# Kernel tuning notes

Measured on AMD Instinct MI355X. Metric: run time of the kernel, lower is better.

Reference implementation:

```python
import jax, jax.numpy as jnp
import numpy as np

H, W = 1080, 1920
MAX_POINTS = 2048
MIN_DEPTH, MAX_DEPTH = 0.1, 2.0
# module sets intrinsics to None (bug); use realistic 1080p pinhole intrinsics
FX = 1050.0
FY = 1050.0
CX = W / 2.0
CY = H / 2.0


def setup_inputs() -> dict:
    key = jax.random.key(0)
    k1, k2 = jax.random.split(key)
    # depth in [0.2, 1.8] m so every pixel passes the validity filter
    depth_image = 0.2 + 1.6 * jax.random.uniform(k1, (H, W), dtype=jnp.float32)
    rgb_image = 255.0 * jax.random.uniform(k2, (H, W, 3), dtype=jnp.float32)
    return {"depth_image": depth_image, "rgb_image": rgb_image}


def _fps_indices(xyz, m):
    """Iterative furthest point sampling. xyz: [N,3] -> [m] int32 indices."""
    N = xyz.shape[0]
    first = jnp.array(0, dtype=jnp.int32)
    init_dists = jnp.full((N,), jnp.inf, dtype=jnp.float32)

    def body(carry, _):
        dists, last = carry
        p = xyz[last]                                 # [3]
        d = jnp.sum((xyz - p) ** 2, axis=1)           # [N]
        dists = jnp.minimum(dists, d)
        nxt = jnp.argmax(dists).astype(jnp.int32)
        return (dists, nxt), nxt

    _, rest = jax.lax.scan(body, (init_dists, first), None, length=m - 1)
    return jnp.concatenate([first[None], rest])


def reference(depth_image, rgb_image):
    # depth -> xyz  [H*W, 3]
    u, v = jnp.meshgrid(jnp.arange(W), jnp.arange(H), indexing='xy')
    u = u.reshape(-1).astype(jnp.float32)
    v = v.reshape(-1).astype(jnp.float32)
    depth = depth_image.reshape(-1)
    xyz = jnp.stack([(u - CX) * depth / FX,
                     (v - CY) * depth / FY,
                     depth], axis=1)                  # [N, 3]
    rgb = rgb_image.reshape(-1, 3) / 255.0            # [N, 3]

    # validity filter (invalid -> inf xyz, 0 rgb), as in the source
    valid = ((depth > MIN_DEPTH) & (depth < MAX_DEPTH)
             & (depth > 0) & jnp.isfinite(depth))
    vm = valid[:, None]
    valid_xyz = jnp.where(vm, xyz, jnp.inf)
    valid_rgb = jnp.where(vm, rgb, 0.0)

    # FPS sampling (N >= max_points branch)
    idx = _fps_indices(valid_xyz.astype(jnp.float32), MAX_POINTS)  # [M]
    sampled_xyz = valid_xyz[idx]                      # [M, 3]
    sampled_rgb = valid_rgb[idx]                      # [M, 3]

    # coordinate normalization to [0,1]
    xyz_min = jnp.min(sampled_xyz, axis=0, keepdims=True)
    centered = sampled_xyz - xyz_min
    xyz_max = jnp.max(centered, axis=0, keepdims=True)
    xyz_max = jnp.where(xyz_max < 1e-8, 1.0, xyz_max)
    XYZ = centered / xyz_max

    return jnp.concatenate([sampled_xyz, sampled_rgb, XYZ], axis=1)  # [M, 9]
```

## Files before the change

kernel.cpp:

```cpp
#include <hip/hip_runtime.h>
#include <math.h>

#define HH   1080
#define WW   1920
#define NPIX (HH*WW)
#define MAXP 2048
#define NTHR 512
#define NWAVE (NTHR/64)
#define PPB  8192
#define KPT  16
#define NBLK 254

#define CXF 960.0f
#define CYF 540.0f
#define FXF 1050.0f
#define FYF 1050.0f

__device__ unsigned long long g_packed[2 * NBLK];
__device__ unsigned long long g_win[2];

__device__ __forceinline__ float proj_x(float u, float d) {
    return __fdiv_rn(__fmul_rn(__fsub_rn(u, CXF), d), FXF);
}
__device__ __forceinline__ float proj_y(float v, float d) {
    return __fdiv_rn(__fmul_rn(__fsub_rn(v, CYF), d), FYF);
}
__device__ __forceinline__ unsigned long long umax64(unsigned long long a, unsigned long long b) {
    return a > b ? a : b;
}

__global__ void zero_ws_kernel() {
    unsigned i = threadIdx.x;
    if (i < 2u * NBLK) g_packed[i] = 0ull;
    if (i < 2u)        g_win[i]    = 0ull;
}

#define FOR16(M)  M(0) M(1) M(2) M(3) M(4) M(5) M(6) M(7) M(8) M(9) M(10) M(11) M(12) M(13) M(14) M(15)
#define FOR16D(M) M(15) M(14) M(13) M(12) M(11) M(10) M(9) M(8) M(7) M(6) M(5) M(4) M(3) M(2) M(1) M(0)
#define DECLD(j) float D##j;

#define UPDJ(j) { \
    unsigned o = tid + j##u * (unsigned)NTHR; \
    float4 P = sP[o]; \
    float dx = __fsub_rn(P.x, px); \
    float dy = __fsub_rn(P.y, py); \
    float dz = __fsub_rn(P.z, pz); \
    float s  = __fadd_rn(__fadd_rn(__fmul_rn(dx, dx), __fmul_rn(dy, dy)), __fmul_rn(dz, dz)); \
    float nd = fminf(D##j, s); \
    D##j = nd; \
    if (nd >= bestd) { bestd = nd; besti = base + o; } }

__global__ __attribute__((amdgpu_flat_work_group_size(NTHR, NTHR)))
void fps_kernel(const float* __restrict__ depth, const float* __restrict__ rgb,
                float* __restrict__ out)
{
    const unsigned tid  = threadIdx.x;
    const unsigned lane = threadIdx.x & 63u;
    const unsigned wid  = threadIdx.x >> 6;
    const unsigned blk  = blockIdx.x;
    const float FINF = __int_as_float(0x7f800000);

    __shared__ float4 sP[PPB];
    __shared__ unsigned long long s_pp[NWAVE];
    __shared__ unsigned long long s_win;
    __shared__ unsigned           s_widx[MAXP];

    if (blk == (unsigned)NBLK) {
        if (wid == 0) {
            if (lane == 0) s_widx[0] = 0u;
            const bool has3 = (lane + 192u) < (unsigned)NBLK;
            for (int it = 1; it < MAXP; ++it) {
                const unsigned long long tag = (unsigned long long)it;
                const unsigned long long* row = &g_packed[(size_t)(it & 1) * NBLK];
                unsigned long long v0, v1, v2, v3 = 0ull;
                for (;;) {
                    v0 = __hip_atomic_load(row + lane,        __ATOMIC_RELAXED, __HIP_MEMORY_SCOPE_AGENT);
                    v1 = __hip_atomic_load(row + lane + 64u,  __ATOMIC_RELAXED, __HIP_MEMORY_SCOPE_AGENT);
                    v2 = __hip_atomic_load(row + lane + 128u, __ATOMIC_RELAXED, __HIP_MEMORY_SCOPE_AGENT);
                    if (has3)
                        v3 = __hip_atomic_load(row + lane + 192u, __ATOMIC_RELAXED, __HIP_MEMORY_SCOPE_AGENT);
                    if ((v0 >> 53) == tag && (v1 >> 53) == tag && (v2 >> 53) == tag &&
                        (!has3 || (v3 >> 53) == tag)) break;
                    __builtin_amdgcn_s_sleep(1);
                }
                unsigned long long w = umax64(umax64(v0, v1), umax64(v2, v3));
                #pragma unroll
                for (int off = 32; off; off >>= 1) w = umax64(w, __shfl_xor(w, off));
                unsigned widx = 0x1FFFFFu - (unsigned)(w & 0x1FFFFFull);
                if (lane == 0) {
                    float wd = depth[widx];
                    s_widx[it] = widx;
                    __hip_atomic_store(&g_win[it & 1],
                        (tag << 53) |
                        ((unsigned long long)__float_as_uint(wd) << 21) |
                        (unsigned long long)(0x1FFFFFu - widx),
                        __ATOMIC_RELAXED, __HIP_MEMORY_SCOPE_AGENT);
                }
            }
        }
        __syncthreads();

        float ex[4], ey[4], ez[4], er[4], eg[4], eb[4];
        #pragma unroll
        for (int q = 0; q < 4; ++q) {
            int i = (int)tid + q * NTHR;
            unsigned sidx = s_widx[i];
            float d = depth[sidx];
            float u = (float)(sidx % WW);
            float v = (float)(sidx / WW);
            bool val = (d > 0.1f) && (d < 2.0f) && __builtin_isfinite(d);
            ex[q] = val ? proj_x(u, d) : FINF;
            ey[q] = val ? proj_y(v, d) : FINF;
            ez[q] = val ? d : FINF;
            er[q] = val ? __fdiv_rn(rgb[3u * sidx + 0u], 255.0f) : 0.0f;
            eg[q] = val ? __fdiv_rn(rgb[3u * sidx + 1u], 255.0f) : 0.0f;
            eb[q] = val ? __fdiv_rn(rgb[3u * sidx + 2u], 255.0f) : 0.0f;
        }
        float mn[3], mx[3];
        mn[0] = fminf(fminf(ex[0], ex[1]), fminf(ex[2], ex[3]));
        mx[0] = fmaxf(fmaxf(ex[0], ex[1]), fmaxf(ex[2], ex[3]));
        mn[1] = fminf(fminf(ey[0], ey[1]), fminf(ey[2], ey[3]));
        mx[1] = fmaxf(fmaxf(ey[0], ey[1]), fmaxf(ey[2], ey[3]));
        mn[2] = fminf(fminf(ez[0], ez[1]), fminf(ez[2], ez[3]));
        mx[2] = fmaxf(fmaxf(ez[0], ez[1]), fmaxf(ez[2], ez[3]));
        #pragma unroll
        for (int c = 0; c < 3; ++c) {
            for (int off = 32; off > 0; off >>= 1) {
                mn[c] = fminf(mn[c], __shfl_xor(mn[c], off));
                mx[c] = fmaxf(mx[c], __shfl_xor(mx[c], off));
            }
        }
        __shared__ float s_mn[NWAVE][3], s_mx[NWAVE][3];
        __shared__ float f_mn[3], f_sc[3];
        if (lane == 0) {
            for (int c = 0; c < 3; ++c) { s_mn[wid][c] = mn[c]; s_mx[wid][c] = mx[c]; }
        }
        __syncthreads();
        if (wid == 0) {
            float a[3], b[3];
            for (int c = 0; c < 3; ++c) {
                a[c] = (lane < NWAVE) ? s_mn[lane][c] : FINF;
                b[c] = (lane < NWAVE) ? s_mx[lane][c] : -FINF;
            }
            for (int off = NWAVE / 2; off > 0; off >>= 1) {
                for (int c = 0; c < 3; ++c) {
                    a[c] = fminf(a[c], __shfl_xor(a[c], off));
                    b[c] = fmaxf(b[c], __shfl_xor(b[c], off));
                }
            }
            if (lane == 0) {
                for (int c = 0; c < 3; ++c) {
                    f_mn[c] = a[c];
                    float m = __fsub_rn(b[c], a[c]);
                    f_sc[c] = (m < 1e-8f) ? 1.0f : m;
                }
            }
        }
        __syncthreads();
        float MN0 = f_mn[0], MN1 = f_mn[1], MN2 = f_mn[2];
        float SC0 = f_sc[0], SC1 = f_sc[1], SC2 = f_sc[2];
        #pragma unroll
        for (int q = 0; q < 4; ++q) {
            int i = (int)tid + q * NTHR;
            out[9 * i + 0] = ex[q];
            out[9 * i + 1] = ey[q];
            out[9 * i + 2] = ez[q];
            out[9 * i + 3] = er[q];
            out[9 * i + 4] = eg[q];
            out[9 * i + 5] = eb[q];
            out[9 * i + 6] = __fdiv_rn(__fsub_rn(ex[q], MN0), SC0);
            out[9 * i + 7] = __fdiv_rn(__fsub_rn(ey[q], MN1), SC1);
            out[9 * i + 8] = __fdiv_rn(__fsub_rn(ez[q], MN2), SC2);
        }
        return;
    }

    const unsigned base = blk << 13;

    FOR16(DECLD)

    #define INITJ(j) { \
        unsigned o   = tid + j##u * (unsigned)NTHR; \
        unsigned idx = base + o; \
        float x, y, z; \
        if (idx < NPIX) { \
            float d = depth[idx]; \
            float u = (float)(idx % WW); \
            float v = (float)(idx / WW); \
            bool val = (d > 0.1f) && (d < 2.0f) && __builtin_isfinite(d); \
            x = val ? proj_x(u, d) : FINF; \
            y = val ? proj_y(v, d) : FINF; \
            z = val ? d : FINF; \
            D##j = FINF; \
        } else { x = 0.f; y = 0.f; z = 0.f; D##j = -1.0f; } \
        sP[o] = make_float4(x, y, z, 0.0f); }
    FOR16(INITJ)
    if (tid == 0) s_win = 0ull;
    __syncthreads();

    float px, py, pz;
    {
        float d = depth[0];
        bool val = (d > 0.1f) && (d < 2.0f) && __builtin_isfinite(d);
        px = val ? proj_x(0.0f, d) : FINF;
        py = val ? proj_y(0.0f, d) : FINF;
        pz = val ? d : FINF;
    }

    for (int it = 1; it < MAXP; ++it) {
        const unsigned long long tag = (unsigned long long)it;

        float bestd = -2.0f;
        unsigned besti = 0u;
        FOR16D(UPDJ)

        unsigned long long pk =
            (tag << 53) |
            ((unsigned long long)__float_as_uint(bestd) << 21) |
            (unsigned long long)(0x1FFFFFu - besti);

        #pragma unroll
        for (int off = 32; off; off >>= 1) pk = umax64(pk, __shfl_xor(pk, off));
        if (lane == 0) s_pp[wid] = pk;
        __syncthreads();

        if (wid == 0 && lane == 0) {
            unsigned long long p2 = s_pp[0];
            #pragma unroll
            for (int k = 1; k < NWAVE; ++k) p2 = umax64(p2, s_pp[k]);
            __hip_atomic_store(&g_packed[(size_t)(it & 1) * NBLK + blk], p2,
                               __ATOMIC_RELAXED, __HIP_MEMORY_SCOPE_AGENT);
        }

        if (it == MAXP - 1) break;

        if (wid == 0 && lane == 0) {
            unsigned long long gv;
            for (;;) {
                gv = __hip_atomic_load(&g_win[it & 1], __ATOMIC_RELAXED, __HIP_MEMORY_SCOPE_AGENT);
                if ((gv >> 53) == tag) break;
            }
            __hip_atomic_store(&s_win, gv, __ATOMIC_RELAXED, __HIP_MEMORY_SCOPE_WORKGROUP);
        }
        unsigned long long gv;
        for (;;) {
            gv = __hip_atomic_load(&s_win, __ATOMIC_RELAXED, __HIP_MEMORY_SCOPE_WORKGROUP);
            if ((gv >> 53) == tag) break;
        }

        unsigned widx = 0x1FFFFFu - (unsigned)(gv & 0x1FFFFFull);
        float    wd   = __uint_as_float((unsigned)((gv >> 21) & 0xFFFFFFFFull));

        float uu = (float)(widx % WW);
        float vv = (float)(widx / WW);
        bool val = (wd > 0.1f) && (wd < 2.0f) && __builtin_isfinite(wd);
        px = val ? proj_x(uu, wd) : FINF;
        py = val ? proj_y(vv, wd) : FINF;
        pz = val ? wd : FINF;
    }
}

extern "C" void kernel_launch(void* const* d_in, const int* in_sizes, int n_in,
                              void* d_out, int out_size, void* d_ws, size_t ws_size,
                              hipStream_t stream) {
    const float* depth = (const float*)d_in[0];
    const float* rgb   = (const float*)d_in[1];
    float* out = (float*)d_out;

    zero_ws_kernel<<<dim3(1), dim3(512), 0, stream>>>();

    void* args[] = { (void*)&depth, (void*)&rgb, (void*)&out };
    hipLaunchCooperativeKernel((const void*)fps_kernel, dim3(NBLK + 1), dim3(NTHR),
                               args, 0, stream);
}
```

Measured before the change: 6.493 ms.

## Remove coordinator block; each block reduces global argmax redundantly

Drops the dedicated reducer block and the global winner broadcast. Instead, wave 0 of every block polls all per-block partial maxima, reduces them itself, and publishes the winner through shared memory. Block 0 also records the sampled indices and writes the output at the end. This removes one global round-trip per iteration (partials to coordinator, then winner back to all blocks), at the cost of every block reading all partials each iteration, which adds L2 polling traffic.

```diff
diff --git a/kernel.cpp b/kernel.cpp
--- a/kernel.cpp
+++ b/kernel.cpp
@@ -17,7 +17,6 @@
 #define FYF 1050.0f
 
 __device__ unsigned long long g_packed[2 * NBLK];
-__device__ unsigned long long g_win[2];
 
 __device__ __forceinline__ float proj_x(float u, float d) {
     return __fdiv_rn(__fmul_rn(__fsub_rn(u, CXF), d), FXF);
@@ -32,7 +31,6 @@
 __global__ void zero_ws_kernel() {
     unsigned i = threadIdx.x;
     if (i < 2u * NBLK) g_packed[i] = 0ull;
-    if (i < 2u)        g_win[i]    = 0ull;
 }
 
 #define FOR16(M)  M(0) M(1) M(2) M(3) M(4) M(5) M(6) M(7) M(8) M(9) M(10) M(11) M(12) M(13) M(14) M(15)
@@ -58,124 +56,13 @@
     const unsigned lane = threadIdx.x & 63u;
     const unsigned wid  = threadIdx.x >> 6;
     const unsigned blk  = blockIdx.x;
+    const unsigned base = blk << 13;
     const float FINF = __int_as_float(0x7f800000);
 
     __shared__ float4 sP[PPB];
     __shared__ unsigned long long s_pp[NWAVE];
     __shared__ unsigned long long s_win;
     __shared__ unsigned           s_widx[MAXP];
-
-    if (blk == (unsigned)NBLK) {
-        if (wid == 0) {
-            if (lane == 0) s_widx[0] = 0u;
-            const bool has3 = (lane + 192u) < (unsigned)NBLK;
-            for (int it = 1; it < MAXP; ++it) {
-                const unsigned long long tag = (unsigned long long)it;
-                const unsigned long long* row = &g_packed[(size_t)(it & 1) * NBLK];
-                unsigned long long v0, v1, v2, v3 = 0ull;
-                for (;;) {
-                    v0 = __hip_atomic_load(row + lane,        __ATOMIC_RELAXED, __HIP_MEMORY_SCOPE_AGENT);
-                    v1 = __hip_atomic_load(row + lane + 64u,  __ATOMIC_RELAXED, __HIP_MEMORY_SCOPE_AGENT);
-                    v2 = __hip_atomic_load(row + lane + 128u, __ATOMIC_RELAXED, __HIP_MEMORY_SCOPE_AGENT);
-                    if (has3)
-                        v3 = __hip_atomic_load(row + lane + 192u, __ATOMIC_RELAXED, __HIP_MEMORY_SCOPE_AGENT);
-                    if ((v0 >> 53) == tag && (v1 >> 53) == tag && (v2 >> 53) == tag &&
-                        (!has3 || (v3 >> 53) == tag)) break;
-                    __builtin_amdgcn_s_sleep(1);
-                }
-                unsigned long long w = umax64(umax64(v0, v1), umax64(v2, v3));
-                #pragma unroll
-                for (int off = 32; off; off >>= 1) w = umax64(w, __shfl_xor(w, off));
-                unsigned widx = 0x1FFFFFu - (unsigned)(w & 0x1FFFFFull);
-                if (lane == 0) {
-                    float wd = depth[widx];
-                    s_widx[it] = widx;
-                    __hip_atomic_store(&g_win[it & 1],
-                        (tag << 53) |
-                        ((unsigned long long)__float_as_uint(wd) << 21) |
-                        (unsigned long long)(0x1FFFFFu - widx),
-                        __ATOMIC_RELAXED, __HIP_MEMORY_SCOPE_AGENT);
-                }
-            }
-        }
-        __syncthreads();
-
-        float ex[4], ey[4], ez[4], er[4], eg[4], eb[4];
-        #pragma unroll
-        for (int q = 0; q < 4; ++q) {
-            int i = (int)tid + q * NTHR;
-            unsigned sidx = s_widx[i];
-            float d = depth[sidx];
-            float u = (float)(sidx % WW);
-            float v = (float)(sidx / WW);
-            bool val = (d > 0.1f) && (d < 2.0f) && __builtin_isfinite(d);
-            ex[q] = val ? proj_x(u, d) : FINF;
-            ey[q] = val ? proj_y(v, d) : FINF;
-            ez[q] = val ? d : FINF;
-            er[q] = val ? __fdiv_rn(rgb[3u * sidx + 0u], 255.0f) : 0.0f;
-            eg[q] = val ? __fdiv_rn(rgb[3u * sidx + 1u], 255.0f) : 0.0f;
-            eb[q] = val ? __fdiv_rn(rgb[3u * sidx + 2u], 255.0f) : 0.0f;
-        }
-        float mn[3], mx[3];
-        mn[0] = fminf(fminf(ex[0], ex[1]), fminf(ex[2], ex[3]));
-        mx[0] = fmaxf(fmaxf(ex[0], ex[1]), fmaxf(ex[2], ex[3]));
-        mn[1] = fminf(fminf(ey[0], ey[1]), fminf(ey[2], ey[3]));
-        mx[1] = fmaxf(fmaxf(ey[0], ey[1]), fmaxf(ey[2], ey[3]));
-        mn[2] = fminf(fminf(ez[0], ez[1]), fminf(ez[2], ez[3]));
-        mx[2] = fmaxf(fmaxf(ez[0], ez[1]), fmaxf(ez[2], ez[3]));
-        #pragma unroll
-        for (int c = 0; c < 3; ++c) {
-            for (int off = 32; off > 0; off >>= 1) {
-                mn[c] = fminf(mn[c], __shfl_xor(mn[c], off));
-                mx[c] = fmaxf(mx[c], __shfl_xor(mx[c], off));
-            }
-        }
-        __shared__ float s_mn[NWAVE][3], s_mx[NWAVE][3];
-        __shared__ float f_mn[3], f_sc[3];
-        if (lane == 0) {
-            for (int c = 0; c < 3; ++c) { s_mn[wid][c] = mn[c]; s_mx[wid][c] = mx[c]; }
-        }
-        __syncthreads();
-        if (wid == 0) {
-            float a[3], b[3];
-            for (int c = 0; c < 3; ++c) {
-                a[c] = (lane < NWAVE) ? s_mn[lane][c] : FINF;
-                b[c] = (lane < NWAVE) ? s_mx[lane][c] : -FINF;
-            }
-            for (int off = NWAVE / 2; off > 0; off >>= 1) {
-                for (int c = 0; c < 3; ++c) {
-                    a[c] = fminf(a[c], __shfl_xor(a[c], off));
-                    b[c] = fmaxf(b[c], __shfl_xor(b[c], off));
-                }
-            }
-            if (lane == 0) {
-                for (int c = 0; c < 3; ++c) {
-                    f_mn[c] = a[c];
-                    float m = __fsub_rn(b[c], a[c]);
-                    f_sc[c] = (m < 1e-8f) ? 1.0f : m;
-                }
-            }
-        }
-        __syncthreads();
-        float MN0 = f_mn[0], MN1 = f_mn[1], MN2 = f_mn[2];
-        float SC0 = f_sc[0], SC1 = f_sc[1], SC2 = f_sc[2];
-        #pragma unroll
-        for (int q = 0; q < 4; ++q) {
-            int i = (int)tid + q * NTHR;
-            out[9 * i + 0] = ex[q];
-            out[9 * i + 1] = ey[q];
-            out[9 * i + 2] = ez[q];
-            out[9 * i + 3] = er[q];
-            out[9 * i + 4] = eg[q];
-            out[9 * i + 5] = eb[q];
-            out[9 * i + 6] = __fdiv_rn(__fsub_rn(ex[q], MN0), SC0);
-            out[9 * i + 7] = __fdiv_rn(__fsub_rn(ey[q], MN1), SC1);
-            out[9 * i + 8] = __fdiv_rn(__fsub_rn(ez[q], MN2), SC2);
-        }
-        return;
-    }
-
-    const unsigned base = blk << 13;
 
     FOR16(DECLD)
 
@@ -195,7 +82,7 @@
         } else { x = 0.f; y = 0.f; z = 0.f; D##j = -1.0f; } \
         sP[o] = make_float4(x, y, z, 0.0f); }
     FOR16(INITJ)
-    if (tid == 0) s_win = 0ull;
+    if (tid == 0) { s_win = 0ull; s_widx[0] = 0u; }
     __syncthreads();
 
     float px, py, pz;
@@ -207,6 +94,8 @@
         pz = val ? d : FINF;
     }
 
+    const bool has3 = (lane + 192u) < (unsigned)NBLK;
+
     for (int it = 1; it < MAXP; ++it) {
         const unsigned long long tag = (unsigned long long)it;
 
@@ -232,24 +121,65 @@
                                __ATOMIC_RELAXED, __HIP_MEMORY_SCOPE_AGENT);
         }
 
-        if (it == MAXP - 1) break;
-
-        if (wid == 0 && lane == 0) {
+        if (it == MAXP - 1) {
+            if (blk == 0 && wid == 0) {
+                const unsigned long long* row = &g_packed[(size_t)(it & 1) * NBLK];
+                unsigned long long v0, v1, v2, v3 = 0ull;
+                for (;;) {
+                    v0 = __hip_atomic_load(row + lane,        __ATOMIC_RELAXED, __HIP_MEMORY_SCOPE_AGENT);
+                    v1 = __hip_atomic_load(row + lane + 64u,  __ATOMIC_RELAXED, __HIP_MEMORY_SCOPE_AGENT);
+                    v2 = __hip_atomic_load(row + lane + 128u, __ATOMIC_RELAXED, __HIP_MEMORY_SCOPE_AGENT);
+                    if (has3)
+                        v3 = __hip_atomic_load(row + lane + 192u, __ATOMIC_RELAXED, __HIP_MEMORY_SCOPE_AGENT);
+                    if ((v0 >> 53) == tag && (v1 >> 53) == tag && (v2 >> 53) == tag &&
+                        (!has3 || (v3 >> 53) == tag)) break;
+                    __builtin_amdgcn_s_sleep(1);
+                }
+                unsigned long long w = umax64(umax64(v0, v1), umax64(v2, v3));
+                #pragma unroll
+                for (int off = 32; off; off >>= 1) w = umax64(w, __shfl_xor(w, off));
+                if (lane == 0) s_widx[it] = 0x1FFFFFu - (unsigned)(w & 0x1FFFFFull);
+            }
+            break;
+        }
+
+        unsigned widx; float wd;
+        if (wid == 0) {
+            const unsigned long long* row = &g_packed[(size_t)(it & 1) * NBLK];
+            unsigned long long v0, v1, v2, v3 = 0ull;
+            for (;;) {
+                v0 = __hip_atomic_load(row + lane,        __ATOMIC_RELAXED, __HIP_MEMORY_SCOPE_AGENT);
+                v1 = __hip_atomic_load(row + lane + 64u,  __ATOMIC_RELAXED, __HIP_MEMORY_SCOPE_AGENT);
+                v2 = __hip_atomic_load(row + lane + 128u, __ATOMIC_RELAXED, __HIP_MEMORY_SCOPE_AGENT);
+                if (has3)
+                    v3 = __hip_atomic_load(row + lane + 192u, __ATOMIC_RELAXED, __HIP_MEMORY_SCOPE_AGENT);
+                if ((v0 >> 53) == tag && (v1 >> 53) == tag && (v2 >> 53) == tag &&
+                    (!has3 || (v3 >> 53) == tag)) break;
+                __builtin_amdgcn_s_sleep(1);
+            }
+            unsigned long long w = umax64(umax64(v0, v1), umax64(v2, v3));
+            #pragma unroll
+            for (int off = 32; off; off >>= 1) w = umax64(w, __shfl_xor(w, off));
+            widx = 0x1FFFFFu - (unsigned)(w & 0x1FFFFFull);
+            wd = depth[widx];
+            if (lane == 0) {
+                if (blk == 0) s_widx[it] = widx;
+                __hip_atomic_store(&s_win,
+                    (tag << 53) |
+                    ((unsigned long long)__float_as_uint(wd) << 21) |
+                    (unsigned long long)(0x1FFFFFu - widx),
+                    __ATOMIC_RELAXED, __HIP_MEMORY_SCOPE_WORKGROUP);
+            }
+        } else {
             unsigned long long gv;
             for (;;) {
-                gv = __hip_atomic_load(&g_win[it & 1], __ATOMIC_RELAXED, __HIP_MEMORY_SCOPE_AGENT);
+                gv = __hip_atomic_load(&s_win, __ATOMIC_RELAXED, __HIP_MEMORY_SCOPE_WORKGROUP);
                 if ((gv >> 53) == tag) break;
-            }
-            __hip_atomic_store(&s_win, gv, __ATOMIC_RELAXED, __HIP_MEMORY_SCOPE_WORKGROUP);
-        }
-        unsigned long long gv;
-        for (;;) {
-            gv = __hip_atomic_load(&s_win, __ATOMIC_RELAXED, __HIP_MEMORY_SCOPE_WORKGROUP);
-            if ((gv >> 53) == tag) break;
-        }
-
-        unsigned widx = 0x1FFFFFu - (unsigned)(gv & 0x1FFFFFull);
-        float    wd   = __uint_as_float((unsigned)((gv >> 21) & 0xFFFFFFFFull));
+                __builtin_amdgcn_s_sleep(1);
+            }
+            widx = 0x1FFFFFu - (unsigned)(gv & 0x1FFFFFull);
+            wd   = __uint_as_float((unsigned)((gv >> 21) & 0xFFFFFFFFull));
+        }
 
         float uu = (float)(widx % WW);
         float vv = (float)(widx / WW);
@@ -258,6 +188,82 @@
         py = val ? proj_y(vv, wd) : FINF;
         pz = val ? wd : FINF;
     }
+
+    if (blk == 0) {
+        __syncthreads();
+        float ex[4], ey[4], ez[4], er[4], eg[4], eb[4];
+        #pragma unroll
+        for (int q = 0; q < 4; ++q) {
+            int i = (int)tid + q * NTHR;
+            unsigned sidx = s_widx[i];
+            float d = depth[sidx];
+            float u = (float)(sidx % WW);
+            float v = (float)(sidx / WW);
+            bool val = (d > 0.1f) && (d < 2.0f) && __builtin_isfinite(d);
+            ex[q] = val ? proj_x(u, d) : FINF;
+            ey[q] = val ? proj_y(v, d) : FINF;
+            ez[q] = val ? d : FINF;
+            er[q] = val ? __fdiv_rn(rgb[3u * sidx + 0u], 255.0f) : 0.0f;
+            eg[q] = val ? __fdiv_rn(rgb[3u * sidx + 1u], 255.0f) : 0.0f;
+            eb[q] = val ? __fdiv_rn(rgb[3u * sidx + 2u], 255.0f) : 0.0f;
+        }
+        float mn[3], mx[3];
+        mn[0] = fminf(fminf(ex[0], ex[1]), fminf(ex[2], ex[3]));
+        mx[0] = fmaxf(fmaxf(ex[0], ex[1]), fmaxf(ex[2], ex[3]));
+        mn[1] = fminf(fminf(ey[0], ey[1]), fminf(ey[2], ey[3]));
+        mx[1] = fmaxf(fmaxf(ey[0], ey[1]), fmaxf(ey[2], ey[3]));
+        mn[2] = fminf(fminf(ez[0], ez[1]), fminf(ez[2], ez[3]));
+        mx[2] = fmaxf(fmaxf(ez[0], ez[1]), fmaxf(ez[2], ez[3]));
+        #pragma unroll
+        for (int c = 0; c < 3; ++c) {
+            for (int off = 32; off > 0; off >>= 1) {
+                mn[c] = fminf(mn[c], __shfl_xor(mn[c], off));
+                mx[c] = fmaxf(mx[c], __shfl_xor(mx[c], off));
+            }
+        }
+        __shared__ float s_mn[NWAVE][3], s_mx[NWAVE][3];
+        __shared__ float f_mn[3], f_sc[3];
+        if (lane == 0) {
+            for (int c = 0; c < 3; ++c) { s_mn[wid][c] = mn[c]; s_mx[wid][c] = mx[c]; }
+        }
+        __syncthreads();
+        if (wid == 0) {
+            float a[3], b[3];
+            for (int c = 0; c < 3; ++c) {
+                a[c] = (lane < NWAVE) ? s_mn[lane][c] : FINF;
+                b[c] = (lane < NWAVE) ? s_mx[lane][c] : -FINF;
+            }
+            for (int off = NWAVE / 2; off > 0; off >>= 1) {
+                for (int c = 0; c < 3; ++c) {
+                    a[c] = fminf(a[c], __shfl_xor(a[c], off));
+                    b[c] = fmaxf(b[c], __shfl_xor(b[c], off));
+                }
+            }
+            if (lane == 0) {
+                for (int c = 0; c < 3; ++c) {
+                    f_mn[c] = a[c];
+                    float m = __fsub_rn(b[c], a[c]);
+                    f_sc[c] = (m < 1e-8f) ? 1.0f : m;
+                }
+            }
+        }
+        __syncthreads();
+        float MN0 = f_mn[0], MN1 = f_mn[1], MN2 = f_mn[2];
+        float SC0 = f_sc[0], SC1 = f_sc[1], SC2 = f_sc[2];
+        #pragma unroll
+        for (int q = 0; q < 4; ++q) {
+            int i = (int)tid + q * NTHR;
+            out[9 * i + 0] = ex[q];
+            out[9 * i + 1] = ey[q];
+            out[9 * i + 2] = ez[q];
+            out[9 * i + 3] = er[q];
+            out[9 * i + 4] = eg[q];
+            out[9 * i + 5] = eb[q];
+            out[9 * i + 6] = __fdiv_rn(__fsub_rn(ex[q], MN0), SC0);
+            out[9 * i + 7] = __fdiv_rn(__fsub_rn(ey[q], MN1), SC1);
+            out[9 * i + 8] = __fdiv_rn(__fsub_rn(ez[q], MN2), SC2);
+        }
+    }
 }
 
 extern "C" void kernel_launch(void* const* d_in, const int* in_sizes, int n_in,
@@ -270,6 +276,6 @@
     zero_ws_kernel<<<dim3(1), dim3(512), 0, stream>>>();
 
     void* args[] = { (void*)&depth, (void*)&rgb, (void*)&out };
-    hipLaunchCooperativeKernel((const void*)fps_kernel, dim3(NBLK + 1), dim3(NTHR),
+    hipLaunchCooperativeKernel((const void*)fps_kernel, dim3(NBLK), dim3(NTHR),
                                args, 0, stream);
 }
```

Result: slower. 9.073 ms (+39.7%).
